# Kernel optimization log

Hardware: AMD Instinct MI355X
Metric: run time of the kernel (lower is better)

Reference implementation:

```python
import jax, jax.numpy as jnp
import numpy as np

N = 512  # n_inputs = n_layers (even)


def setup_inputs() -> dict:
    key = jax.random.key(0)
    ks = jax.random.split(key, 8)
    H = N // 2
    two_pi = 2.0 * np.pi
    return {
        "thetas_full": jax.random.uniform(ks[0], (N, N), jnp.float32, 0.0, two_pi),
        "thetas_inout": jax.random.uniform(ks[1], (2, N), jnp.float32, 0.0, two_pi),
        "pc_losses_full": 0.05 * jax.random.uniform(ks[2], (N, N), jnp.float32),
        "pc_losses_inout": 0.05 * jax.random.uniform(ks[3], (2, N), jnp.float32),
        "mmi_losses_even": 0.05 * jax.random.uniform(ks[4], (N, H), jnp.float32),
        "mmi_losses_odd": 0.05 * jax.random.uniform(ks[5], (N, H - 1), jnp.float32),
        "mmi_imb_even": jax.random.uniform(ks[6], (N, H), jnp.float32, -0.05, 0.05),
        "mmi_imb_odd": jax.random.uniform(ks[7], (N, H - 1), jnp.float32, -0.05, 0.05),
    }


def _pc(M, theta, loss):
    # diag(sqrt(1-loss) * exp(i*theta)) @ M  -- phase shifter on every waveguide
    a = jnp.sqrt(1.0 - loss) * jnp.exp(1j * theta)  # complex64 [n]
    return a[:, None] * M


def _mmi_pairs(top, bot, loss, imb):
    # 2x2 MMI coupler sqrt(1-loss) * [[t, i r], [i r, t]], t=sqrt(.5+imb), r=sqrt(.5-imb)
    a = jnp.sqrt(1.0 - loss)[:, None]
    t = (a * jnp.sqrt(0.5 + imb)[:, None]).astype(top.dtype)
    r = (a * jnp.sqrt(0.5 - imb)[:, None])
    ir = (1j * r).astype(top.dtype)
    return t * top + ir * bot, ir * top + t * bot


def _mmi_even(M, loss, imb):
    # couplers on row pairs (0,1),(2,3),...
    n = M.shape[0]
    P = M.reshape(n // 2, 2, n)
    top, bot = _mmi_pairs(P[:, 0], P[:, 1], loss, imb)
    return jnp.stack([top, bot], axis=1).reshape(n, n)


def _mmi_odd(M, loss, imb):
    # couplers on row pairs (1,2),(3,4),...; rows 0 and n-1 pass through
    n = M.shape[0]
    P = M[1:-1].reshape(n // 2 - 1, 2, n)
    top, bot = _mmi_pairs(P[:, 0], P[:, 1], loss, imb)
    inner = jnp.stack([top, bot], axis=1).reshape(n - 2, n)
    return jnp.concatenate([M[:1], inner, M[-1:]], axis=0)


def _forward(thetas_full, thetas_inout, pc_losses_full, pc_losses_inout,
             mmi_losses_even, mmi_losses_odd, mmi_imb_even, mmi_imb_odd):
    n = thetas_full.shape[1]
    h = n // 2
    M = jnp.eye(n, dtype=jnp.complex64)
    M = _pc(M, thetas_inout[0], pc_losses_inout[0])
    # pack params two layers per scan step (loop body uses indices 2i and 2i+1)
    xs = (thetas_full.reshape(h, 2, n), pc_losses_full.reshape(h, 2, n),
          mmi_losses_even.reshape(h, 2, h), mmi_imb_even.reshape(h, 2, h),
          mmi_losses_odd.reshape(h, 2, h - 1), mmi_imb_odd.reshape(h, 2, h - 1))

    def step(M, x):
        th, lp, le, ie, lo, io = x
        M = _mmi_even(M, le[0], ie[0])
        M = _pc(M, th[0], lp[0])
        M = _mmi_even(M, le[1], ie[1])
        M = _mmi_odd(M, lo[0], io[0])
        M = _pc(M, th[1], lp[1])
        M = _mmi_odd(M, lo[1], io[1])
        return M, None

    M, _ = jax.lax.scan(jax.checkpoint(step), M, xs)
    return _pc(M, thetas_inout[1], pc_losses_inout[1])


def reference(thetas_full, thetas_inout, pc_losses_full, pc_losses_inout,
              mmi_losses_even, mmi_losses_odd, mmi_imb_even, mmi_imb_odd):
    return _forward(thetas_full, thetas_inout, pc_losses_full, pc_losses_inout,
                    mmi_losses_even, mmi_losses_odd, mmi_imb_even, mmi_imb_odd)
```

## Files before the change

### kernel.cpp

```cpp
#include <hip/hip_runtime.h>
#include <math.h>

#define NROWS   512
#define NSTEPS  256
#define PKSTEPS (NSTEPS + 2)

__device__ float4 g_pk[PKSTEPS * 5 * 256];
__device__ float2 g_io[1024];


__device__ __forceinline__ float2 pc_coef(float th, float loss) {
  float a = sqrtf(1.0f - loss);
  float s, c;
  sincosf(th, &s, &c);
  return make_float2(a * c, a * s);
}
__device__ __forceinline__ float2 mmi_coef(float loss, float imb) {
  float a = sqrtf(1.0f - loss);
  return make_float2(a * sqrtf(0.5f + imb), a * sqrtf(0.5f - imb));
}

__global__ void precomp_kernel(const float* __restrict__ thf,
                               const float* __restrict__ thio,
                               const float* __restrict__ lpf,
                               const float* __restrict__ lpio,
                               const float* __restrict__ le,
                               const float* __restrict__ lo,
                               const float* __restrict__ ie,
                               const float* __restrict__ io2) {
  const int b   = blockIdx.x;
  const int tid = threadIdx.x;
  if (b >= NSTEPS) {
    int j = (b - NSTEPS) * 256 + tid;
    g_io[j]       = pc_coef(thio[j],       lpio[j]);
    g_io[j + 512] = pc_coef(thio[j + 512], lpio[j + 512]);
    return;
  }
  const int i  = b;
  const int w  = tid >> 6, l = tid & 63;
  const int R0 = 128 * w + 2 * l;
  const int p  = 64 * w + l;
  const int L0 = 2 * i, L1 = 2 * i + 1;

  float2 e0  = mmi_coef(le[L0 * 256 + p], ie[L0 * 256 + p]);
  float2 e1  = mmi_coef(le[L1 * 256 + p], ie[L1 * 256 + p]);
  float2 p0a = pc_coef(thf[L0 * 512 + R0],     lpf[L0 * 512 + R0]);
  float2 p0b = pc_coef(thf[L0 * 512 + R0 + 1], lpf[L0 * 512 + R0 + 1]);
  float2 p1a = pc_coef(thf[L1 * 512 + R0],     lpf[L1 * 512 + R0]);
  float2 p1b = pc_coef(thf[L1 * 512 + R0 + 1], lpf[L1 * 512 + R0 + 1]);
  float2 one = make_float2(1.0f, 0.0f);
  float2 o0T = (p <= 254) ? mmi_coef(lo[L0 * 255 + p],     io2[L0 * 255 + p])     : one;
  float2 o0B = (p >= 1)   ? mmi_coef(lo[L0 * 255 + p - 1], io2[L0 * 255 + p - 1]) : one;
  float2 o1T = (p <= 254) ? mmi_coef(lo[L1 * 255 + p],     io2[L1 * 255 + p])     : one;
  float2 o1B = (p >= 1)   ? mmi_coef(lo[L1 * 255 + p - 1], io2[L1 * 255 + p - 1]) : one;

  float4* base = g_pk + (i * 5) * 256 + tid;
  base[0]        = make_float4(e0.x,  e0.y,  e1.x,  e1.y);
  base[256]      = make_float4(p0a.x, p0a.y, p0b.x, p0b.y);
  base[2 * 256]  = make_float4(o0T.x, o0T.y, o0B.x, o0B.y);
  base[3 * 256]  = make_float4(p1a.x, p1a.y, p1b.x, p1b.y);
  base[4 * 256]  = make_float4(o1T.x, o1T.y, o1B.x, o1B.y);
}


__device__ __forceinline__ void cmul(float2& v, float ar, float ai) {
  float xr = ar * v.x - ai * v.y;
  float xi = ar * v.y + ai * v.x;
  v.x = xr; v.y = xi;
}
__device__ __forceinline__ void mmix(float2& top, float2& bot, float t, float r) {
  float a = t * top.x - r * bot.y;
  float b = t * top.y + r * bot.x;
  float c = t * bot.x - r * top.y;
  float d = t * bot.y + r * top.x;
  top.x = a; top.y = b; bot.x = c; bot.y = d;
}
__device__ __forceinline__ void upd(float2& v, float t, float r, float2 o) {
  float xr = t * v.x - r * o.y;
  float xi = t * v.y + r * o.x;
  v.x = xr; v.y = xi;
}

__global__ __launch_bounds__(256) void prop_kernel(float* __restrict__ out,
                                                   int write_complex) {
  __shared__ float2 sUp[2][2][4];
  __shared__ float2 sDn[2][2][4];
  const int tid = threadIdx.x;
  const int l = tid & 63, w = tid >> 6;
  const int R0 = 128 * w + 2 * l;
  const int colbase = blockIdx.x * 2;

  float2 v[2][2];
  #pragma unroll
  for (int c = 0; c < 2; ++c)
    #pragma unroll
    for (int k = 0; k < 2; ++k)
      v[c][k] = (colbase + c == R0 + k) ? make_float2(1.0f, 0.0f)
                                        : make_float2(0.0f, 0.0f);

  auto odd = [&](float4 c, int sid) {
    float2 nb0, nb1, pt0, pt1;
    nb0.x = __shfl_down(v[0][0].x, 1); nb0.y = __shfl_down(v[0][0].y, 1);
    nb1.x = __shfl_down(v[1][0].x, 1); nb1.y = __shfl_down(v[1][0].y, 1);
    pt0.x = __shfl_up(v[0][1].x, 1);   pt0.y = __shfl_up(v[0][1].y, 1);
    pt1.x = __shfl_up(v[1][1].x, 1);   pt1.y = __shfl_up(v[1][1].y, 1);
    if (l == 0)  { sDn[0][sid][w] = v[0][0]; sDn[1][sid][w] = v[1][0]; }
    if (l == 63) { sUp[0][sid][w] = v[0][1]; sUp[1][sid][w] = v[1][1]; }
    __syncthreads();
    if (l == 63 && w < 3) { nb0 = sDn[0][sid][w + 1]; nb1 = sDn[1][sid][w + 1]; }
    if (l == 0 && w > 0)  { pt0 = sUp[0][sid][w - 1]; pt1 = sUp[1][sid][w - 1]; }
    if (!(w == 3 && l == 63)) {
      upd(v[0][1], c.x, c.y, nb0);
      upd(v[1][1], c.x, c.y, nb1);
    }
    if (!(w == 0 && l == 0)) {
      upd(v[0][0], c.z, c.w, pt0);
      upd(v[1][0], c.z, c.w, pt1);
    }
  };

  auto step = [&](float4 f0, float4 f1, float4 f2, float4 f3, float4 f4) {
    mmix(v[0][0], v[0][1], f0.x, f0.y);
    mmix(v[1][0], v[1][1], f0.x, f0.y);
    cmul(v[0][0], f1.x, f1.y); cmul(v[1][0], f1.x, f1.y);
    cmul(v[0][1], f1.z, f1.w); cmul(v[1][1], f1.z, f1.w);
    mmix(v[0][0], v[0][1], f0.z, f0.w);
    mmix(v[1][0], v[1][1], f0.z, f0.w);
    odd(f2, 0);
    cmul(v[0][0], f3.x, f3.y); cmul(v[1][0], f3.x, f3.y);
    cmul(v[0][1], f3.z, f3.w); cmul(v[1][1], f3.z, f3.w);
    odd(f4, 1);
  };

  {
    float4 a = *(const float4*)(g_io + R0);
    cmul(v[0][0], a.x, a.y); cmul(v[1][0], a.x, a.y);
    cmul(v[0][1], a.z, a.w); cmul(v[1][1], a.z, a.w);
  }

  const float4* P = g_pk + tid;
  float4 a0 = P[0],        a1 = P[256],        a2 = P[512],
         a3 = P[768],      a4 = P[1024];
  float4 b0 = P[1280],     b1 = P[1280+256],   b2 = P[1280+512],
         b3 = P[1280+768], b4 = P[1280+1024];

  #pragma unroll 1
  for (int i = 0; i < NSTEPS; i += 2) {
    const float4* Q = P + (i + 2) * 1280;
    float4 n0 = Q[0], n1 = Q[256], n2 = Q[512], n3 = Q[768], n4 = Q[1024];
    step(a0, a1, a2, a3, a4);
    a0 = n0; a1 = n1; a2 = n2; a3 = n3; a4 = n4;
    const float4* R = P + (i + 3) * 1280;
    n0 = R[0]; n1 = R[256]; n2 = R[512]; n3 = R[768]; n4 = R[1024];
    step(b0, b1, b2, b3, b4);
    b0 = n0; b1 = n1; b2 = n2; b3 = n3; b4 = n4;
  }

  {
    float4 a = *(const float4*)(g_io + 512 + R0);
    cmul(v[0][0], a.x, a.y); cmul(v[1][0], a.x, a.y);
    cmul(v[0][1], a.z, a.w); cmul(v[1][1], a.z, a.w);
  }

  if (write_complex) {
    float2* o = (float2*)out;
    #pragma unroll
    for (int c = 0; c < 2; ++c) {
      o[(R0 + 0) * NROWS + colbase + c] = v[c][0];
      o[(R0 + 1) * NROWS + colbase + c] = v[c][1];
    }
  } else {
    #pragma unroll
    for (int c = 0; c < 2; ++c) {
      out[(R0 + 0) * NROWS + colbase + c] = v[c][0].x;
      out[(R0 + 1) * NROWS + colbase + c] = v[c][1].x;
    }
  }
}


extern "C" void kernel_launch(void* const* d_in, const int* in_sizes, int n_in,
                              void* d_out, int out_size, void* d_ws, size_t ws_size,
                              hipStream_t stream) {
  const float* thf  = (const float*)d_in[0];
  const float* thio = (const float*)d_in[1];
  const float* lpf  = (const float*)d_in[2];
  const float* lpio = (const float*)d_in[3];
  const float* le   = (const float*)d_in[4];
  const float* lo   = (const float*)d_in[5];
  const float* ie   = (const float*)d_in[6];
  const float* io2  = (const float*)d_in[7];

  const int write_complex = (out_size >= 2 * NROWS * NROWS) ? 1 : 0;

  precomp_kernel<<<NSTEPS + 2, 256, 0, stream>>>(
      thf, thio, lpf, lpio, le, lo, ie, io2);
  prop_kernel<<<NROWS / 2, 256, 0, stream>>>((float*)d_out, write_complex);
}
```

Measured before the change: 220.1 us.

## Shrink per-step coefficient stream and replicate coefficient table across blocks

Packs each step's coefficients into four float4 per thread instead of five. The bottom odd-coupler coefficient is no longer stored; it is fetched from the neighbouring lane with a shuffle, and wave-boundary lanes do one extra load. The coefficient table is also written in eight copies, and blocks pick a copy by block index, which spreads L2/global traffic across more addresses. This trades extra precompute writes and a few shuffles per step for less load bandwidth in the serial propagation loop.

```diff
diff --git a/kernel.cpp b/kernel.cpp
--- a/kernel.cpp
+++ b/kernel.cpp
@@ -4,8 +4,10 @@
 #define NROWS   512
 #define NSTEPS  256
 #define PKSTEPS (NSTEPS + 2)
-
-__device__ float4 g_pk[PKSTEPS * 5 * 256];
+#define PKF4    1024
+#define NREP    8
+
+__device__ float4 g_pk[NREP][PKSTEPS * PKF4];
 __device__ float2 g_io[1024];
 
 
@@ -49,17 +51,22 @@
   float2 p1a = pc_coef(thf[L1 * 512 + R0],     lpf[L1 * 512 + R0]);
   float2 p1b = pc_coef(thf[L1 * 512 + R0 + 1], lpf[L1 * 512 + R0 + 1]);
   float2 one = make_float2(1.0f, 0.0f);
-  float2 o0T = (p <= 254) ? mmi_coef(lo[L0 * 255 + p],     io2[L0 * 255 + p])     : one;
-  float2 o0B = (p >= 1)   ? mmi_coef(lo[L0 * 255 + p - 1], io2[L0 * 255 + p - 1]) : one;
-  float2 o1T = (p <= 254) ? mmi_coef(lo[L1 * 255 + p],     io2[L1 * 255 + p])     : one;
-  float2 o1B = (p >= 1)   ? mmi_coef(lo[L1 * 255 + p - 1], io2[L1 * 255 + p - 1]) : one;
-
-  float4* base = g_pk + (i * 5) * 256 + tid;
-  base[0]        = make_float4(e0.x,  e0.y,  e1.x,  e1.y);
-  base[256]      = make_float4(p0a.x, p0a.y, p0b.x, p0b.y);
-  base[2 * 256]  = make_float4(o0T.x, o0T.y, o0B.x, o0B.y);
-  base[3 * 256]  = make_float4(p1a.x, p1a.y, p1b.x, p1b.y);
-  base[4 * 256]  = make_float4(o1T.x, o1T.y, o1B.x, o1B.y);
+  float2 o0T = (p <= 254) ? mmi_coef(lo[L0 * 255 + p], io2[L0 * 255 + p]) : one;
+  float2 o1T = (p <= 254) ? mmi_coef(lo[L1 * 255 + p], io2[L1 * 255 + p]) : one;
+
+  float4 F0 = make_float4(e0.x,  e0.y,  e1.x,  e1.y);
+  float4 F1 = make_float4(p0a.x, p0a.y, p0b.x, p0b.y);
+  float4 F2 = make_float4(o0T.x, o0T.y, o1T.x, o1T.y);
+  float4 F3 = make_float4(p1a.x, p1a.y, p1b.x, p1b.y);
+
+  #pragma unroll
+  for (int r = 0; r < NREP; ++r) {
+    float4* base = &g_pk[r][i * PKF4] + tid;
+    base[0]       = F0;
+    base[256]     = F1;
+    base[2 * 256] = F2;
+    base[3 * 256] = F3;
+  }
 }
 
 
@@ -89,6 +96,8 @@
   const int l = tid & 63, w = tid >> 6;
   const int R0 = 128 * w + 2 * l;
   const int colbase = blockIdx.x * 2;
+  const int rep = blockIdx.x & (NREP - 1);
+  const bool haveB = (l == 0 && w > 0);
 
   float2 v[2][2];
   #pragma unroll
@@ -98,7 +107,7 @@
       v[c][k] = (colbase + c == R0 + k) ? make_float2(1.0f, 0.0f)
                                         : make_float2(0.0f, 0.0f);
 
-  auto odd = [&](float4 c, int sid) {
+  auto odd = [&](float ctx, float cty, float cbex, float cbey, int sid) {
     float2 nb0, nb1, pt0, pt1;
     nb0.x = __shfl_down(v[0][0].x, 1); nb0.y = __shfl_down(v[0][0].y, 1);
     nb1.x = __shfl_down(v[1][0].x, 1); nb1.y = __shfl_down(v[1][0].y, 1);
@@ -109,27 +118,30 @@
     __syncthreads();
     if (l == 63 && w < 3) { nb0 = sDn[0][sid][w + 1]; nb1 = sDn[1][sid][w + 1]; }
     if (l == 0 && w > 0)  { pt0 = sUp[0][sid][w - 1]; pt1 = sUp[1][sid][w - 1]; }
+    float cbx = __shfl_up(ctx, 1);
+    float cby = __shfl_up(cty, 1);
+    if (haveB) { cbx = cbex; cby = cbey; }
     if (!(w == 3 && l == 63)) {
-      upd(v[0][1], c.x, c.y, nb0);
-      upd(v[1][1], c.x, c.y, nb1);
+      upd(v[0][1], ctx, cty, nb0);
+      upd(v[1][1], ctx, cty, nb1);
     }
     if (!(w == 0 && l == 0)) {
-      upd(v[0][0], c.z, c.w, pt0);
-      upd(v[1][0], c.z, c.w, pt1);
+      upd(v[0][0], cbx, cby, pt0);
+      upd(v[1][0], cbx, cby, pt1);
     }
   };
 
-  auto step = [&](float4 f0, float4 f1, float4 f2, float4 f3, float4 f4) {
+  auto step = [&](float4 f0, float4 f1, float4 f2, float4 f3, float4 fB) {
     mmix(v[0][0], v[0][1], f0.x, f0.y);
     mmix(v[1][0], v[1][1], f0.x, f0.y);
     cmul(v[0][0], f1.x, f1.y); cmul(v[1][0], f1.x, f1.y);
     cmul(v[0][1], f1.z, f1.w); cmul(v[1][1], f1.z, f1.w);
     mmix(v[0][0], v[0][1], f0.z, f0.w);
     mmix(v[1][0], v[1][1], f0.z, f0.w);
-    odd(f2, 0);
+    odd(f2.x, f2.y, fB.x, fB.y, 0);
     cmul(v[0][0], f3.x, f3.y); cmul(v[1][0], f3.x, f3.y);
     cmul(v[0][1], f3.z, f3.w); cmul(v[1][1], f3.z, f3.w);
-    odd(f4, 1);
+    odd(f2.z, f2.w, fB.z, fB.w, 1);
   };
 
   {
@@ -138,22 +150,27 @@
     cmul(v[0][1], a.z, a.w); cmul(v[1][1], a.z, a.w);
   }
 
-  const float4* P = g_pk + tid;
-  float4 a0 = P[0],        a1 = P[256],        a2 = P[512],
-         a3 = P[768],      a4 = P[1024];
-  float4 b0 = P[1280],     b1 = P[1280+256],   b2 = P[1280+512],
-         b3 = P[1280+768], b4 = P[1280+1024];
+  const float4* P = &g_pk[rep][0] + tid;
+  float4 zero = make_float4(1.0f, 0.0f, 1.0f, 0.0f);
+  float4 a0 = P[0],    a1 = P[256],       a2 = P[512],       a3 = P[768];
+  float4 b0 = P[PKF4], b1 = P[PKF4+256],  b2 = P[PKF4+512],  b3 = P[PKF4+768];
+  float4 aB = zero, bB = zero;
+  if (haveB) { aB = P[511]; bB = P[PKF4 + 511]; }
 
   #pragma unroll 1
   for (int i = 0; i < NSTEPS; i += 2) {
-    const float4* Q = P + (i + 2) * 1280;
-    float4 n0 = Q[0], n1 = Q[256], n2 = Q[512], n3 = Q[768], n4 = Q[1024];
-    step(a0, a1, a2, a3, a4);
-    a0 = n0; a1 = n1; a2 = n2; a3 = n3; a4 = n4;
-    const float4* R = P + (i + 3) * 1280;
-    n0 = R[0]; n1 = R[256]; n2 = R[512]; n3 = R[768]; n4 = R[1024];
-    step(b0, b1, b2, b3, b4);
-    b0 = n0; b1 = n1; b2 = n2; b3 = n3; b4 = n4;
+    const float4* Q = P + (i + 2) * PKF4;
+    float4 n0 = Q[0], n1 = Q[256], n2 = Q[512], n3 = Q[768];
+    float4 nB = zero;
+    if (haveB) nB = Q[511];
+    step(a0, a1, a2, a3, aB);
+    a0 = n0; a1 = n1; a2 = n2; a3 = n3; aB = nB;
+    const float4* R = P + (i + 3) * PKF4;
+    n0 = R[0]; n1 = R[256]; n2 = R[512]; n3 = R[768];
+    nB = zero;
+    if (haveB) nB = R[511];
+    step(b0, b1, b2, b3, bB);
+    b0 = n0; b1 = n1; b2 = n2; b3 = n3; bB = nB;
   }
 
   {
```

Measured after the change: 256.5 us. 1.17x slower.
